# Performance work log

Hardware: AMD Instinct MI355X
Metric: run time of the kernel (lower is better)

The kernel has to match this reference:

```python
import jax, jax.numpy as jnp
import numpy as np

B, IMG, IND, E, FF = 64, 1024, 64, 4, 16
LN_EPS = 1e-5


def _layernorm(x, g, b):
    m = x.mean(-1, keepdims=True)
    v = ((x - m) ** 2).mean(-1, keepdims=True)
    return (x - m) / jnp.sqrt(v + LN_EPS) * g + b


def _encoder_layer(x, qkv_w, qkv_b, o_w, o_b, ln1_g, ln1_b,
                   ff1_w, ff1_b, ff2_w, ff2_b, ln2_g, ln2_b):
    # Post-norm TransformerEncoderLayer (nhead=1, relu, dropout inactive at eval)
    qkv = x @ qkv_w + qkv_b                      # [B,S,3E]
    q, k, v = jnp.split(qkv, 3, axis=-1)
    scores = jnp.einsum('bsd,btd->bst', q, k) / jnp.sqrt(jnp.float32(E))
    a = jax.nn.softmax(scores, axis=-1)
    attn = jnp.einsum('bst,btd->bsd', a, v) @ o_w + o_b
    x = _layernorm(x + attn, ln1_g, ln1_b)
    ff = jax.nn.relu(x @ ff1_w + ff1_b) @ ff2_w + ff2_b
    x = _layernorm(x + ff, ln2_g, ln2_b)
    return x


def setup_inputs() -> dict:
    ks = iter(jax.random.split(jax.random.key(0), 64))

    def nrm(shape, s=0.1):
        return jax.random.normal(next(ks), shape, jnp.float32) * s

    inp = {
        'image_embeds': nrm((B, IMG, 1), 1.0),
        'indicator_embeds': nrm((B, 1, IND), 1.0),
        'w_in1': nrm((1, E)), 'b_in1': nrm((E,)),
        'w_in2': nrm((1, E)), 'b_in2': nrm((E,)),
        'w_out1': nrm((E, 1)), 'b_out1': nrm((1,)),
        'w_out2': nrm((E, 1)), 'b_out2': nrm((1,)),
    }
    for p in ('t1', 't2'):
        inp[f'{p}_qkv_w'] = nrm((E, 3 * E)); inp[f'{p}_qkv_b'] = nrm((3 * E,))
        inp[f'{p}_o_w'] = nrm((E, E)); inp[f'{p}_o_b'] = nrm((E,))
        inp[f'{p}_ln1_g'] = jnp.ones((E,), jnp.float32); inp[f'{p}_ln1_b'] = jnp.zeros((E,), jnp.float32)
        inp[f'{p}_ff1_w'] = nrm((E, FF)); inp[f'{p}_ff1_b'] = nrm((FF,))
        inp[f'{p}_ff2_w'] = nrm((FF, E)); inp[f'{p}_ff2_b'] = nrm((E,))
        inp[f'{p}_ln2_g'] = jnp.ones((E,), jnp.float32); inp[f'{p}_ln2_b'] = jnp.zeros((E,), jnp.float32)
    inp['w_cls'] = nrm((IMG + IND, 3))
    inp['b_cls'] = nrm((3,))
    return inp


def reference(image_embeds, indicator_embeds,
              w_in1, b_in1, w_in2, b_in2, w_out1, b_out1, w_out2, b_out2,
              t1_qkv_w, t1_qkv_b, t1_o_w, t1_o_b, t1_ln1_g, t1_ln1_b,
              t1_ff1_w, t1_ff1_b, t1_ff2_w, t1_ff2_b, t1_ln2_g, t1_ln2_b,
              t2_qkv_w, t2_qkv_b, t2_o_w, t2_o_b, t2_ln1_g, t2_ln1_b,
              t2_ff1_w, t2_ff1_b, t2_ff2_w, t2_ff2_b, t2_ln2_g, t2_ln2_b,
              w_cls, b_cls):
    ind = jnp.swapaxes(indicator_embeds, 1, 2)   # [B, IND, 1]
    img = image_embeds @ w_in1 + b_in1           # [B, IMG, E]
    img = _encoder_layer(img, t1_qkv_w, t1_qkv_b, t1_o_w, t1_o_b,
                         t1_ln1_g, t1_ln1_b, t1_ff1_w, t1_ff1_b,
                         t1_ff2_w, t1_ff2_b, t1_ln2_g, t1_ln2_b)
    img = img @ w_out1 + b_out1                  # [B, IMG, 1]
    ind = ind @ w_in2 + b_in2                    # [B, IND, E]
    ind = _encoder_layer(ind, t2_qkv_w, t2_qkv_b, t2_o_w, t2_o_b,
                         t2_ln1_g, t2_ln1_b, t2_ff1_w, t2_ff1_b,
                         t2_ff2_w, t2_ff2_b, t2_ln2_g, t2_ln2_b)
    ind = ind @ w_out2 + b_out2                  # [B, IND, 1]
    x = jnp.concatenate((img, ind), axis=1)[..., 0]  # [B, IMG+IND]
    x = x @ w_cls + b_cls                        # [B, 3]
    return jax.nn.softmax(x, axis=-1)
```

## Files before the change

kernel.cpp:

```cpp
#include <hip/hip_runtime.h>

#define B_    64
#define IMG_  1024
#define IND_  64
#define NTHR  256
#define IMG_BPB 16

enum {
  W_IN = 0, B_IN = 4, QKV_W = 8, QKV_B = 56, O_W = 68, O_B = 84,
  LN1G = 88, LN1B = 92, FF1W = 96, FF1B = 160, FF2W = 176, FF2B = 240,
  LN2G = 244, LN2B = 248, W_OUT = 252, B_OUT = 256, WTOT = 257
};

struct KArgs {
  const float* in[36];
  float* ws_img;
  float* ws_ind;
};

__device__ __forceinline__ void stage(float* dst, const float* src, int n, int tid) {
  for (int i = tid; i < n; i += NTHR) dst[i] = src[i];
}

__global__ __launch_bounds__(NTHR) void fused_enc(KArgs A) {
  const int blk = blockIdx.x;
  const int tid = threadIdx.x;
  const bool is_img = blk < B_ * IMG_BPB;

  __shared__ float w[WTOT];
  __shared__ float iv[IMG_];

  int batch, row, S, tb;
  const float* xin;
  if (is_img) {
    batch = blk >> 4; row = ((blk & 15) << 6) + (tid >> 2); S = IMG_;
    xin = A.in[0] + batch * IMG_; tb = 10;
  } else {
    batch = blk - B_ * IMG_BPB; row = tid >> 2; S = IND_;
    xin = A.in[1] + batch * IND_; tb = 22;
  }

  stage(w + W_IN,  A.in[is_img ? 2 : 4], 4,  tid);
  stage(w + B_IN,  A.in[is_img ? 3 : 5], 4,  tid);
  stage(w + W_OUT, A.in[is_img ? 6 : 8], 4,  tid);
  stage(w + B_OUT, A.in[is_img ? 7 : 9], 1,  tid);
  stage(w + QKV_W, A.in[tb + 0], 48, tid);
  stage(w + QKV_B, A.in[tb + 1], 12, tid);
  stage(w + O_W,   A.in[tb + 2], 16, tid);
  stage(w + O_B,   A.in[tb + 3], 4,  tid);
  stage(w + LN1G,  A.in[tb + 4], 4,  tid);
  stage(w + LN1B,  A.in[tb + 5], 4,  tid);
  stage(w + FF1W,  A.in[tb + 6], 64, tid);
  stage(w + FF1B,  A.in[tb + 7], 16, tid);
  stage(w + FF2W,  A.in[tb + 8], 64, tid);
  stage(w + FF2B,  A.in[tb + 9], 4,  tid);
  stage(w + LN2G,  A.in[tb + 10], 4, tid);
  stage(w + LN2B,  A.in[tb + 11], 4, tid);
  for (int i = tid; i < S; i += NTHR) iv[i] = xin[i];
  __syncthreads();

  float qd[4], qb[4], kd[4], kb[4], vd[4], vb[4];
#pragma unroll
  for (int j = 0; j < 4; j++) {
    float a0 = 0.f, a1 = 0.f, a2 = 0.f, b0 = 0.f, b1 = 0.f, b2 = 0.f;
#pragma unroll
    for (int e = 0; e < 4; e++) {
      const float we = w[W_IN + e], be = w[B_IN + e];
      a0 += we * w[QKV_W + e * 12 + j];      b0 += be * w[QKV_W + e * 12 + j];
      a1 += we * w[QKV_W + e * 12 + 4 + j];  b1 += be * w[QKV_W + e * 12 + 4 + j];
      a2 += we * w[QKV_W + e * 12 + 8 + j];  b2 += be * w[QKV_W + e * 12 + 8 + j];
    }
    qd[j] = a0; qb[j] = b0 + w[QKV_B + j];
    kd[j] = a1; kb[j] = b1 + w[QKV_B + 4 + j];
    vd[j] = a2; vb[j] = b2 + w[QKV_B + 8 + j];
  }
  float c1 = 0.f, c0 = 0.f;
#pragma unroll
  for (int j = 0; j < 4; j++) { c1 += qd[j] * kd[j]; c0 += qb[j] * kd[j]; }
  float HB[4], HC[4];
#pragma unroll
  for (int j = 0; j < 4; j++) {
    float s1 = 0.f, s2 = 0.f;
#pragma unroll
    for (int f = 0; f < 4; f++) {
      s1 += vd[f] * w[O_W + f * 4 + j];
      s2 += vb[f] * w[O_W + f * 4 + j];
    }
    HB[j] = s1; HC[j] = w[B_IN + j] + s2 + w[O_B + j];
  }

  const float ivr = iv[row];
  const float ah = 0.5f * 1.4426950408889634f * (c1 * ivr + c0);

  const int c = tid & 3;
  const int nch = S >> 2;
  float S0 = 0.f, S1 = 0.f;
  for (int ci = c; ci < nch; ci += 4) {
    const float4 t4 = *reinterpret_cast<const float4*>(&iv[ci << 2]);
    float p;
    p = exp2f(ah * t4.x); S0 += p; S1 = fmaf(p, t4.x, S1);
    p = exp2f(ah * t4.y); S0 += p; S1 = fmaf(p, t4.y, S1);
    p = exp2f(ah * t4.z); S0 += p; S1 = fmaf(p, t4.z, S1);
    p = exp2f(ah * t4.w); S0 += p; S1 = fmaf(p, t4.w, S1);
  }
  S0 += __shfl_xor(S0, 1); S1 += __shfl_xor(S1, 1);
  S0 += __shfl_xor(S0, 2); S1 += __shfl_xor(S1, 2);
  const float rho = S1 / S0;

  float h[4];
#pragma unroll
  for (int j = 0; j < 4; j++) h[j] = w[W_IN + j] * ivr + HB[j] * rho + HC[j];
  {
    const float m = 0.25f * (h[0] + h[1] + h[2] + h[3]);
    float v = 0.f;
#pragma unroll
    for (int j = 0; j < 4; j++) { const float d = h[j] - m; v += d * d; }
    const float rs = rsqrtf(v * 0.25f + 1e-5f);
#pragma unroll
    for (int j = 0; j < 4; j++) h[j] = (h[j] - m) * rs * w[LN1G + j] + w[LN1B + j];
  }
  float f2[4] = {w[FF2B + 0], w[FF2B + 1], w[FF2B + 2], w[FF2B + 3]};
#pragma unroll
  for (int t = 0; t < 16; t++) {
    float u = w[FF1B + t];
#pragma unroll
    for (int j = 0; j < 4; j++) u += h[j] * w[FF1W + j * 16 + t];
    u = fmaxf(u, 0.f);
#pragma unroll
    for (int j = 0; j < 4; j++) f2[j] += u * w[FF2W + t * 4 + j];
  }
  float h2[4];
#pragma unroll
  for (int j = 0; j < 4; j++) h2[j] = h[j] + f2[j];
  {
    const float m = 0.25f * (h2[0] + h2[1] + h2[2] + h2[3]);
    float v = 0.f;
#pragma unroll
    for (int j = 0; j < 4; j++) { const float d = h2[j] - m; v += d * d; }
    const float rs = rsqrtf(v * 0.25f + 1e-5f);
#pragma unroll
    for (int j = 0; j < 4; j++) h2[j] = (h2[j] - m) * rs * w[LN2G + j] + w[LN2B + j];
  }
  float out = w[B_OUT];
#pragma unroll
  for (int j = 0; j < 4; j++) out += h2[j] * w[W_OUT + j];

  if (c == 0) {
    if (is_img) A.ws_img[batch * IMG_ + row] = out;
    else        A.ws_ind[batch * IND_ + row] = out;
  }
}

__global__ __launch_bounds__(256) void cls_head(const float* __restrict__ img_o,
                                                const float* __restrict__ ind_o,
                                                const float* __restrict__ w_cls,
                                                const float* __restrict__ b_cls,
                                                float* __restrict__ out) {
  const int b = blockIdx.x, tid = threadIdx.x;
  float p0 = 0.f, p1 = 0.f, p2 = 0.f;
  const float* xi = img_o + b * IMG_;
  for (int i = tid; i < IMG_; i += 256) {
    const float v = xi[i];
    p0 += v * w_cls[i * 3 + 0];
    p1 += v * w_cls[i * 3 + 1];
    p2 += v * w_cls[i * 3 + 2];
  }
  if (tid < IND_) {
    const float v = ind_o[b * IND_ + tid];
    const int j = IMG_ + tid;
    p0 += v * w_cls[j * 3 + 0];
    p1 += v * w_cls[j * 3 + 1];
    p2 += v * w_cls[j * 3 + 2];
  }
  for (int off = 32; off > 0; off >>= 1) {
    p0 += __shfl_down(p0, off, 64);
    p1 += __shfl_down(p1, off, 64);
    p2 += __shfl_down(p2, off, 64);
  }
  __shared__ float red[4][3];
  if ((tid & 63) == 0) { const int wv = tid >> 6; red[wv][0] = p0; red[wv][1] = p1; red[wv][2] = p2; }
  __syncthreads();
  if (tid == 0) {
    float z0 = red[0][0] + red[1][0] + red[2][0] + red[3][0] + b_cls[0];
    float z1 = red[0][1] + red[1][1] + red[2][1] + red[3][1] + b_cls[1];
    float z2 = red[0][2] + red[1][2] + red[2][2] + red[3][2] + b_cls[2];
    const float mx = fmaxf(z0, fmaxf(z1, z2));
    const float e0 = __expf(z0 - mx), e1 = __expf(z1 - mx), e2 = __expf(z2 - mx);
    const float rs = 1.f / (e0 + e1 + e2);
    out[b * 3 + 0] = e0 * rs;
    out[b * 3 + 1] = e1 * rs;
    out[b * 3 + 2] = e2 * rs;
  }
}

extern "C" void kernel_launch(void* const* d_in, const int* in_sizes, int n_in,
                              void* d_out, int out_size, void* d_ws, size_t ws_size,
                              hipStream_t stream) {
  KArgs A;
  for (int i = 0; i < 36; i++) A.in[i] = (const float*)d_in[i];
  A.ws_img = (float*)d_ws;
  A.ws_ind = A.ws_img + B_ * IMG_;

  fused_enc<<<B_ * IMG_BPB + B_, NTHR, 0, stream>>>(A);
  cls_head<<<B_, 256, 0, stream>>>(A.ws_img, A.ws_ind, A.in[34], A.in[35],
                                   (float*)d_out);
}
```

Baseline: 151.2 us.

## Fuse classifier head into encoder kernel via atomics and last-block softmax

Drops the separate classifier kernel. Each block now multiplies its per-row outputs by w_cls, reduces them across the block, and atomically adds the partial logits into a per-batch accumulator. The last block to finish, found with a ticket counter, applies the bias and softmax. This removes the second launch and the workspace round trip, but adds a memset, contended float atomics on 192 addresses and a nondeterministic summation order. It also drops the unused k-bias computation.

```diff
diff --git a/kernel.cpp b/kernel.cpp
--- a/kernel.cpp
+++ b/kernel.cpp
@@ -5,6 +5,7 @@
 #define IND_  64
 #define NTHR  256
 #define IMG_BPB 16
+#define NBLK  (B_ * IMG_BPB + B_)
 
 enum {
   W_IN = 0, B_IN = 4, QKV_W = 8, QKV_B = 56, O_W = 68, O_B = 84,
@@ -14,21 +15,24 @@
 
 struct KArgs {
   const float* in[36];
-  float* ws_img;
-  float* ws_ind;
+  float* acc;
+  unsigned int* cnt;
+  float* out;
 };
 
 __device__ __forceinline__ void stage(float* dst, const float* src, int n, int tid) {
   for (int i = tid; i < n; i += NTHR) dst[i] = src[i];
 }
 
-__global__ __launch_bounds__(NTHR) void fused_enc(KArgs A) {
+__global__ __launch_bounds__(NTHR) void fused_all(KArgs A) {
   const int blk = blockIdx.x;
   const int tid = threadIdx.x;
   const bool is_img = blk < B_ * IMG_BPB;
 
   __shared__ float w[WTOT];
   __shared__ float iv[IMG_];
+  __shared__ float red[4][3];
+  __shared__ unsigned int sticket;
 
   int batch, row, S, tb;
   const float* xin;
@@ -39,6 +43,7 @@
     batch = blk - B_ * IMG_BPB; row = tid >> 2; S = IND_;
     xin = A.in[1] + batch * IND_; tb = 22;
   }
+  const int g = is_img ? row : (IMG_ + row);
 
   stage(w + W_IN,  A.in[is_img ? 2 : 4], 4,  tid);
   stage(w + B_IN,  A.in[is_img ? 3 : 5], 4,  tid);
@@ -59,19 +64,19 @@
   for (int i = tid; i < S; i += NTHR) iv[i] = xin[i];
   __syncthreads();
 
-  float qd[4], qb[4], kd[4], kb[4], vd[4], vb[4];
+  float qd[4], qb[4], kd[4], vd[4], vb[4];
 #pragma unroll
   for (int j = 0; j < 4; j++) {
-    float a0 = 0.f, a1 = 0.f, a2 = 0.f, b0 = 0.f, b1 = 0.f, b2 = 0.f;
+    float a0 = 0.f, a1 = 0.f, a2 = 0.f, b0 = 0.f, b2 = 0.f;
 #pragma unroll
     for (int e = 0; e < 4; e++) {
       const float we = w[W_IN + e], be = w[B_IN + e];
       a0 += we * w[QKV_W + e * 12 + j];      b0 += be * w[QKV_W + e * 12 + j];
-      a1 += we * w[QKV_W + e * 12 + 4 + j];  b1 += be * w[QKV_W + e * 12 + 4 + j];
+      a1 += we * w[QKV_W + e * 12 + 4 + j];
       a2 += we * w[QKV_W + e * 12 + 8 + j];  b2 += be * w[QKV_W + e * 12 + 8 + j];
     }
     qd[j] = a0; qb[j] = b0 + w[QKV_B + j];
-    kd[j] = a1; kb[j] = b1 + w[QKV_B + 4 + j];
+    kd[j] = a1;
     vd[j] = a2; vb[j] = b2 + w[QKV_B + 8 + j];
   }
   float c1 = 0.f, c0 = 0.f;
@@ -145,51 +150,42 @@
 #pragma unroll
   for (int j = 0; j < 4; j++) out += h2[j] * w[W_OUT + j];
 
+  float p0 = 0.f, p1 = 0.f, p2 = 0.f;
   if (c == 0) {
-    if (is_img) A.ws_img[batch * IMG_ + row] = out;
-    else        A.ws_ind[batch * IND_ + row] = out;
-  }
-}
-
-__global__ __launch_bounds__(256) void cls_head(const float* __restrict__ img_o,
-                                                const float* __restrict__ ind_o,
-                                                const float* __restrict__ w_cls,
-                                                const float* __restrict__ b_cls,
-                                                float* __restrict__ out) {
-  const int b = blockIdx.x, tid = threadIdx.x;
-  float p0 = 0.f, p1 = 0.f, p2 = 0.f;
-  const float* xi = img_o + b * IMG_;
-  for (int i = tid; i < IMG_; i += 256) {
-    const float v = xi[i];
-    p0 += v * w_cls[i * 3 + 0];
-    p1 += v * w_cls[i * 3 + 1];
-    p2 += v * w_cls[i * 3 + 2];
-  }
-  if (tid < IND_) {
-    const float v = ind_o[b * IND_ + tid];
-    const int j = IMG_ + tid;
-    p0 += v * w_cls[j * 3 + 0];
-    p1 += v * w_cls[j * 3 + 1];
-    p2 += v * w_cls[j * 3 + 2];
-  }
-  for (int off = 32; off > 0; off >>= 1) {
-    p0 += __shfl_down(p0, off, 64);
-    p1 += __shfl_down(p1, off, 64);
-    p2 += __shfl_down(p2, off, 64);
-  }
-  __shared__ float red[4][3];
-  if ((tid & 63) == 0) { const int wv = tid >> 6; red[wv][0] = p0; red[wv][1] = p1; red[wv][2] = p2; }
+    const float* wc = A.in[34] + 3 * g;
+    p0 = out * wc[0]; p1 = out * wc[1]; p2 = out * wc[2];
+  }
+#pragma unroll
+  for (int m = 1; m < 64; m <<= 1) {
+    p0 += __shfl_xor(p0, m); p1 += __shfl_xor(p1, m); p2 += __shfl_xor(p2, m);
+  }
+  if ((tid & 63) == 0) {
+    const int wv = tid >> 6;
+    red[wv][0] = p0; red[wv][1] = p1; red[wv][2] = p2;
+  }
   __syncthreads();
   if (tid == 0) {
-    float z0 = red[0][0] + red[1][0] + red[2][0] + red[3][0] + b_cls[0];
-    float z1 = red[0][1] + red[1][1] + red[2][1] + red[3][1] + b_cls[1];
-    float z2 = red[0][2] + red[1][2] + red[2][2] + red[3][2] + b_cls[2];
-    const float mx = fmaxf(z0, fmaxf(z1, z2));
-    const float e0 = __expf(z0 - mx), e1 = __expf(z1 - mx), e2 = __expf(z2 - mx);
-    const float rs = 1.f / (e0 + e1 + e2);
-    out[b * 3 + 0] = e0 * rs;
-    out[b * 3 + 1] = e1 * rs;
-    out[b * 3 + 2] = e2 * rs;
+    atomicAdd(&A.acc[batch * 3 + 0], red[0][0] + red[1][0] + red[2][0] + red[3][0]);
+    atomicAdd(&A.acc[batch * 3 + 1], red[0][1] + red[1][1] + red[2][1] + red[3][1]);
+    atomicAdd(&A.acc[batch * 3 + 2], red[0][2] + red[1][2] + red[2][2] + red[3][2]);
+    __threadfence();
+    sticket = atomicAdd(A.cnt, 1u);
+  }
+  __syncthreads();
+
+  if (sticket == NBLK - 1) {
+    __threadfence();
+    if (tid < B_) {
+      const float z0 = atomicAdd(&A.acc[tid * 3 + 0], 0.0f) + A.in[35][0];
+      const float z1 = atomicAdd(&A.acc[tid * 3 + 1], 0.0f) + A.in[35][1];
+      const float z2 = atomicAdd(&A.acc[tid * 3 + 2], 0.0f) + A.in[35][2];
+      const float mx = fmaxf(z0, fmaxf(z1, z2));
+      const float e0 = __expf(z0 - mx), e1 = __expf(z1 - mx), e2 = __expf(z2 - mx);
+      const float rs = 1.f / (e0 + e1 + e2);
+      A.out[tid * 3 + 0] = e0 * rs;
+      A.out[tid * 3 + 1] = e1 * rs;
+      A.out[tid * 3 + 2] = e2 * rs;
+    }
   }
 }
 
@@ -198,10 +194,10 @@
                               hipStream_t stream) {
   KArgs A;
   for (int i = 0; i < 36; i++) A.in[i] = (const float*)d_in[i];
-  A.ws_img = (float*)d_ws;
-  A.ws_ind = A.ws_img + B_ * IMG_;
-
-  fused_enc<<<B_ * IMG_BPB + B_, NTHR, 0, stream>>>(A);
-  cls_head<<<B_, 256, 0, stream>>>(A.ws_img, A.ws_ind, A.in[34], A.in[35],
-                                   (float*)d_out);
+  A.acc = (float*)d_ws;
+  A.cnt = (unsigned int*)((float*)d_ws + 192);
+  A.out = (float*)d_out;
+
+  hipMemsetAsync(d_ws, 0, 1024, stream);
+  fused_all<<<NBLK, NTHR, 0, stream>>>(A);
 }
```

Result: slower. 158.2 us (+4.7%).
